# Kernel optimization log

Hardware: AMD Instinct MI355X
Metric: run time of the kernel (lower is better)

The kernel has to match this reference:

```python
import jax, jax.numpy as jnp
import numpy as np

B, H, N, D = 16, 8, 256, 32


def setup_inputs() -> dict:
    key = jax.random.key(0)
    k1, k2, k3 = jax.random.split(key, 3)
    q = jax.random.normal(k1, (B, H, N, D), dtype=jnp.float32)
    k = jax.random.normal(k2, (B, H, N, D), dtype=jnp.float32)
    scale = jnp.ones((1,), dtype=jnp.float32)  # unused by the module
    mask = jnp.zeros((B, 1, N, N), dtype=bool)  # True == masked out
    # learned attention vector, xavier_uniform over (1, H, 1, 1, D)
    fan = 1 * H * 1 * 1 * D
    bound = float(np.sqrt(6.0 / (1 + D)))  # xavier for (..., D) param
    attention = jax.random.uniform(k3, (1, H, 1, 1, D), dtype=jnp.float32,
                                   minval=-bound, maxval=bound)
    return {"q": q, "k": k, "scale": scale, "mask": mask, "attention": attention}


def reference(q, k, scale, mask, attention):
    # summed: [B, H, Nq, Nk, D] via broadcast of q.unsqueeze(-2)+k.unsqueeze(-3)
    summed = q[:, :, :, None, :] + k[:, :, None, :, :]
    # GATv2 score: a^T * silu(q_i + k_j), reduced over head_dim
    scores = jnp.sum(jax.nn.silu(summed) * attention, axis=-1)  # [B, H, Nq, Nk]
    neg = jnp.finfo(scores.dtype).min
    scores_masked = jnp.where(mask, neg, scores)
    attn = jax.nn.softmax(scores_masked, axis=-1)
    return attn
```

## Files before the change

kernel.cpp:

```cpp
#include <hip/hip_runtime.h>
#include <stdint.h>
#include <stddef.h>

constexpr int Bc = 16, Hc = 8, Nc = 256, Dc = 32;
constexpr float LOG2E = 1.44269504088896340736f;

constexpr int    MF    = 10;
constexpr double PHALF = 9.7;
constexpr double LFIT  = 9.0;

constexpr double PI_ = 3.14159265358979323846;

constexpr double cexp_(double x) {
    int n = (int)(x >= 0 ? x + 0.5 : x - 0.5);
    double f = x - n, t = 1.0, s = 1.0;
    for (int i = 1; i <= 26; ++i) { t *= f / i; s += t; }
    const double E = 2.71828182845904523536;
    double en = 1.0, bb = n >= 0 ? E : 1.0 / E;
    int an = n < 0 ? -n : n;
    for (int i = 0; i < an; ++i) en *= bb;
    return s * en;
}
constexpr double creduce_(double x) {
    while (x >  PI_) x -= 2.0 * PI_;
    while (x < -PI_) x += 2.0 * PI_;
    return x;
}
constexpr double ccos_(double x0) {
    double x = creduce_(x0), x2 = x * x, t = 1.0, s = 1.0;
    for (int i = 1; i <= 16; ++i) { t *= -x2 / ((2.0*i - 1.0) * (2.0*i)); s += t; }
    return s;
}
constexpr double csin_(double x0) {
    double x = creduce_(x0), x2 = x * x, t = x, s = x;
    for (int i = 1; i <= 16; ++i) { t *= -x2 / ((2.0*i) * (2.0*i + 1.0)); s += t; }
    return s;
}
constexpr double Gfun_(double x) {
    double z = x < 0 ? -x : x;
    double e = cexp_(z);
    return 0.5 * z * ((e - 1.0) / (e + 1.0));
}
constexpr double csqrt_(double x) {
    if (x <= 0) return 0;
    double r = x > 1 ? x : 1;
    for (int i = 0; i < 40; ++i) r = 0.5 * (r + x / r);
    return r;
}

struct FitT { float tk[MF + 1]; float tq[MF + 1]; };

constexpr FitT lsFit_() {
    constexpr int NB = MF + 1;
    double A[NB][NB] = {}, bv[NB] = {};
    for (int p = 0; p < NB; ++p)
        for (int qq = 0; qq < NB; ++qq) {
            double wm = (p - qq) * PI_ / PHALF, wp = (p + qq) * PI_ / PHALF;
            double Sm = (p == qq)     ? LFIT : csin_(wm * LFIT) / wm;
            double Sp = (p + qq == 0) ? LFIT : csin_(wp * LFIT) / wp;
            A[p][qq] = 0.5 * (Sm + Sp);
        }
    constexpr int NS = 128;
    double hh = LFIT / NS, gx[NS + 1] = {};
    for (int i = 0; i <= NS; ++i) gx[i] = Gfun_(i * hh);
    for (int p = 0; p < NB; ++p) {
        double s = 0;
        for (int i = 0; i <= NS; ++i) {
            double wgt = (i == 0 || i == NS) ? 1.0 : ((i & 1) ? 4.0 : 2.0);
            s += wgt * gx[i] * ccos_(p * PI_ / PHALF * (i * hh));
        }
        bv[p] = s * hh / 3.0;
    }
    for (int p = 0; p < NB; ++p) A[p][p] += 1e-8 * LFIT;
    for (int col = 0; col < NB; ++col) {
        int piv = col; double best = A[col][col] < 0 ? -A[col][col] : A[col][col];
        for (int r = col + 1; r < NB; ++r) {
            double v = A[r][col] < 0 ? -A[r][col] : A[r][col];
            if (v > best) { best = v; piv = r; }
        }
        if (piv != col) {
            for (int cc = 0; cc < NB; ++cc) { double t = A[col][cc]; A[col][cc] = A[piv][cc]; A[piv][cc] = t; }
            double t = bv[col]; bv[col] = bv[piv]; bv[piv] = t;
        }
        for (int r = col + 1; r < NB; ++r) {
            double f = A[r][col] / A[col][col];
            for (int cc = col; cc < NB; ++cc) A[r][cc] -= f * A[col][cc];
            bv[r] -= f * bv[col];
        }
    }
    double c[NB] = {};
    for (int r = NB - 1; r >= 0; --r) {
        double s = bv[r];
        for (int cc = r + 1; cc < NB; ++cc) s -= A[r][cc] * c[cc];
        c[r] = s / A[r][r];
    }
    FitT f{};
    for (int m = 0; m <= MF; ++m) {
        double rt = csqrt_(c[m] < 0 ? -c[m] : c[m]);
        f.tk[m] = (float)rt;
        f.tq[m] = (float)(c[m] < 0 ? -rt : rt);
    }
    return f;
}
constexpr FitT CF = lsFit_();

typedef _Float16 half8  __attribute__((ext_vector_type(8)));
typedef float    f32x16 __attribute__((ext_vector_type(16)));

__device__ __forceinline__ uint32_t pkh_(float a, float b) {
    auto v = __builtin_amdgcn_cvt_pkrtz(a, b);
    uint32_t u; __builtin_memcpy(&u, &v, 4); return u;
}

constexpr int KB_  = Nc * 128;
constexpr int QB_  = 128 * 128;
constexpr int BUF  = KB_ + QB_;
constexpr int SRED_OFF = 2 * BUF;
constexpr int AKV_OFF  = SRED_OFF + 2048;
constexpr int SMEM     = AKV_OFF + 1024;

__global__ __launch_bounds__(1024, 4) void gatv2_mfma_kernel(
    const float* __restrict__ q, const float* __restrict__ k,
    const uint8_t* __restrict__ mask, const float* __restrict__ att,
    float* __restrict__ out)
{
    extern __shared__ char smem[];
    float* sred = (float*)(smem + SRED_OFF);
    float* akv  = (float*)(smem + AKV_OFF);

    const int tid = threadIdx.x, lane = tid & 63, w = tid >> 6;
    const int bh = blockIdx.y, h = bh & 7, b = bh >> 3;
    const int iBlk = blockIdx.x * 128;
    const float invTwoP = (float)(1.0 / (2.0 * PHALF));

    const int dq = tid & 7, rw = tid >> 3;
    const float4 a4 = *(const float4*)(att + h * Dc + 4 * dq);
    const int swS = (dq ^ (rw & 7)) << 4;

    const float* kbase = k + (size_t)bh * Nc * Dc;
    float kc1[8], ks1[8], kcm[8], ksm[8];
    int offK[2];
#pragma unroll
    for (int it = 0; it < 2; ++it) {
        const int j = rw + it * 128;
        const float4 kv = *(const float4*)(kbase + j * Dc + 4 * dq);
        float part = a4.x * kv.x + a4.y * kv.y + a4.z * kv.z + a4.w * kv.w;
        part += __shfl_xor(part, 1, 64);
        part += __shfl_xor(part, 2, 64);
        part += __shfl_xor(part, 4, 64);
        if (dq == 0) akv[j] = part;
        const float rv[4] = { kv.x, kv.y, kv.z, kv.w };
#pragma unroll
        for (int c = 0; c < 4; ++c) {
            float r = __builtin_amdgcn_fractf(rv[c] * invTwoP);
            kc1[4*it+c] = __builtin_amdgcn_cosf(r);
            ks1[4*it+c] = __builtin_amdgcn_sinf(r);
            kcm[4*it+c] = kc1[4*it+c];
            ksm[4*it+c] = ks1[4*it+c];
        }
        offK[it] = j * 128 + swS;
    }
    const float* qbase = q + ((size_t)bh * Nc + iBlk) * Dc;
    float qc1[4], qs1[4], qcm[4], qsm[4];
    const int offQ = KB_ + rw * 128 + swS;
    {
        const float4 qv = *(const float4*)(qbase + rw * Dc + 4 * dq);
        const float rv[4] = { qv.x, qv.y, qv.z, qv.w };
#pragma unroll
        for (int c = 0; c < 4; ++c) {
            float r = __builtin_amdgcn_fractf(rv[c] * invTwoP);
            qc1[c] = __builtin_amdgcn_cosf(r);
            qs1[c] = __builtin_amdgcn_sinf(r);
            qcm[c] = qc1[c]; qsm[c] = qs1[c];
        }
    }

    const int hi5 = lane >> 5, col = lane & 31;
    const int wi = w & 3, wj = w >> 2;
    const int baseA  = KB_ + (wi * 32 + col) * 128;
    const int baseB0 = (wj * 64 + col) * 128, baseB1 = baseB0 + 32 * 128;
    const int sA = col & 7;

    f32x16 acc[2];
#pragma unroll
    for (int jt = 0; jt < 2; ++jt)
#pragma unroll
        for (int e = 0; e < 16; ++e) acc[jt][e] = 0.0f;

    auto buildChunk = [&](int m, int dstOff) {
        const float tk = CF.tk[m];
        const float g0 = CF.tq[m]*a4.x, g1 = CF.tq[m]*a4.y;
        const float g2 = CF.tq[m]*a4.z, g3 = CF.tq[m]*a4.w;
#pragma unroll
        for (int it = 0; it < 2; ++it) {
            uint4 wv;
            wv.x = pkh_(tk * kcm[4*it+0], tk * ksm[4*it+0]);
            wv.y = pkh_(tk * kcm[4*it+1], tk * ksm[4*it+1]);
            wv.z = pkh_(tk * kcm[4*it+2], tk * ksm[4*it+2]);
            wv.w = pkh_(tk * kcm[4*it+3], tk * ksm[4*it+3]);
            *(uint4*)(smem + dstOff + offK[it]) = wv;
        }
        {
            uint4 wv;
            wv.x = pkh_(g0 * qcm[0], -(g0 * qsm[0]));
            wv.y = pkh_(g1 * qcm[1], -(g1 * qsm[1]));
            wv.z = pkh_(g2 * qcm[2], -(g2 * qsm[2]));
            wv.w = pkh_(g3 * qcm[3], -(g3 * qsm[3]));
            *(uint4*)(smem + dstOff + offQ) = wv;
        }
        if (m < MF) {
#pragma unroll
            for (int e = 0; e < 8; ++e) {
                float cn = fmaf(kc1[e], kcm[e], -(ks1[e] * ksm[e]));
                float sn = fmaf(ks1[e], kcm[e],   kc1[e] * ksm[e]);
                kcm[e] = cn; ksm[e] = sn;
            }
#pragma unroll
            for (int e = 0; e < 4; ++e) {
                float cn = fmaf(qc1[e], qcm[e], -(qs1[e] * qsm[e]));
                float sn = fmaf(qs1[e], qcm[e],   qc1[e] * qsm[e]);
                qcm[e] = cn; qsm[e] = sn;
            }
        }
    };

    auto mfmaChunk = [&](int srcOff) {
#pragma unroll
        for (int s = 0; s < 4; ++s) {
            const int du = ((2 * s + hi5) ^ sA) << 4;
            half8 A  = *(const half8*)(smem + srcOff + baseA  + du);
            half8 B0 = *(const half8*)(smem + srcOff + baseB0 + du);
            half8 B1 = *(const half8*)(smem + srcOff + baseB1 + du);
            acc[0] = __builtin_amdgcn_mfma_f32_32x32x16_f16(A, B0, acc[0], 0, 0, 0);
            acc[1] = __builtin_amdgcn_mfma_f32_32x32x16_f16(A, B1, acc[1], 0, 0, 0);
        }
    };

    buildChunk(1, 0);
    __syncthreads();
#pragma unroll
    for (int m = 1; m <= MF; ++m) {
        if (m < MF) buildChunk(m + 1, (m & 1) * BUF);
        mfmaChunk(((m - 1) & 1) * BUF);
        __syncthreads();
    }

    constexpr float M0 = 24.0f;
    const int jB = wj * 64;
    const float akj0 = akv[jB + col], akj1 = akv[jB + 32 + col];
    const int iB = iBlk + wi * 32;

#pragma unroll
    for (int e = 0; e < 16; ++e) {
        int rloc = (e & 3) + 8 * (e >> 2) + 4 * hi5;
        int ig = iB + rloc;
        const uint8_t* mr = mask + ((size_t)(b * Nc + ig)) * Nc + jB + col;
        float v0 = fmaf(0.5f, akj0, acc[0][e]);
        float v1 = fmaf(0.5f, akj1, acc[1][e]);
        if (mr[0])  v0 = -1.0e30f;
        if (mr[32]) v1 = -1.0e30f;
        float p0 = __builtin_amdgcn_exp2f(__builtin_fminf((v0 - M0) * LOG2E, 80.0f));
        float p1 = __builtin_amdgcn_exp2f(__builtin_fminf((v1 - M0) * LOG2E, 80.0f));
        acc[0][e] = p0;
        acc[1][e] = p1;
        float sm = p0 + p1;
#pragma unroll
        for (int off = 1; off < 32; off <<= 1) sm += __shfl_xor(sm, off, 64);
        if (col == e) sred[(wi * 32 + rloc) * 4 + wj] = sm;
    }
    __syncthreads();

    float* obase = out + (size_t)bh * Nc * Nc;
#pragma unroll
    for (int e = 0; e < 16; ++e) {
        int rloc = (e & 3) + 8 * (e >> 2) + 4 * hi5;
        int iL = wi * 32 + rloc;
        int ig = iB + rloc;
        float4 tv = *(const float4*)(&sred[iL * 4]);
        float inv = __builtin_amdgcn_rcpf(tv.x + tv.y + tv.z + tv.w);
        obase[(size_t)ig * Nc + jB + col]      = acc[0][e] * inv;
        obase[(size_t)ig * Nc + jB + 32 + col] = acc[1][e] * inv;
    }
}

extern "C" void kernel_launch(void* const* d_in, const int* in_sizes, int n_in,
                              void* d_out, int out_size, void* d_ws, size_t ws_size,
                              hipStream_t stream) {
    const float*   q    = (const float*)d_in[0];
    const float*   k    = (const float*)d_in[1];
    const uint8_t* mask = (const uint8_t*)d_in[3];
    const float*   att  = (const float*)d_in[4];
    float*         out  = (float*)d_out;

    (void)hipFuncSetAttribute((const void*)gatv2_mfma_kernel,
                              hipFuncAttributeMaxDynamicSharedMemorySize, SMEM);

    dim3 grid(2, Bc * Hc);
    dim3 block(1024);
    gatv2_mfma_kernel<<<grid, block, SMEM, stream>>>(q, k, mask, att, out);
}
```

Before: 97.27 us.

## Split blocks into 64-row tiles with 512 threads and direct per-harmonic sincos

Halves the query tile per block (64 rows, 512 threads, grid 4x128) so more blocks exist and LDS per block drops. Each thread now handles four key rows. Sin/cos of each harmonic are computed directly from the fractional phase instead of through the angle-addition recurrence, which frees registers. The akv and row-sum scratch space now reuses the Q buffer after the main loop. The cost is that every K row's fp16 chunk is rebuilt by twice as many blocks, and there are more transcendental instructions per chunk.

```diff
diff --git a/kernel.cpp b/kernel.cpp
--- a/kernel.cpp
+++ b/kernel.cpp
@@ -112,25 +112,21 @@
     uint32_t u; __builtin_memcpy(&u, &v, 4); return u;
 }
 
-constexpr int KB_  = Nc * 128;
-constexpr int QB_  = 128 * 128;
-constexpr int BUF  = KB_ + QB_;
-constexpr int SRED_OFF = 2 * BUF;
-constexpr int AKV_OFF  = SRED_OFF + 2048;
-constexpr int SMEM     = AKV_OFF + 1024;
-
-__global__ __launch_bounds__(1024, 4) void gatv2_mfma_kernel(
+constexpr int KHALF = Nc * 128;
+constexpr int QOFF  = 2 * KHALF;
+constexpr int QHALF = 64 * 128;
+constexpr int SMEM  = QOFF + 2 * QHALF;
+
+__global__ __launch_bounds__(512, 4) void gatv2_mfma_kernel(
     const float* __restrict__ q, const float* __restrict__ k,
     const uint8_t* __restrict__ mask, const float* __restrict__ att,
     float* __restrict__ out)
 {
     extern __shared__ char smem[];
-    float* sred = (float*)(smem + SRED_OFF);
-    float* akv  = (float*)(smem + AKV_OFF);
 
     const int tid = threadIdx.x, lane = tid & 63, w = tid >> 6;
     const int bh = blockIdx.y, h = bh & 7, b = bh >> 3;
-    const int iBlk = blockIdx.x * 128;
+    const int iBlk = blockIdx.x * 64;
     const float invTwoP = (float)(1.0 / (2.0 * PHALF));
 
     const int dq = tid & 7, rw = tid >> 3;
@@ -138,47 +134,39 @@
     const int swS = (dq ^ (rw & 7)) << 4;
 
     const float* kbase = k + (size_t)bh * Nc * Dc;
-    float kc1[8], ks1[8], kcm[8], ksm[8];
-    int offK[2];
-#pragma unroll
-    for (int it = 0; it < 2; ++it) {
-        const int j = rw + it * 128;
+    float r1k[16], akvr[4];
+    int offK[4];
+#pragma unroll
+    for (int it = 0; it < 4; ++it) {
+        const int j = rw + it * 64;
         const float4 kv = *(const float4*)(kbase + j * Dc + 4 * dq);
         float part = a4.x * kv.x + a4.y * kv.y + a4.z * kv.z + a4.w * kv.w;
         part += __shfl_xor(part, 1, 64);
         part += __shfl_xor(part, 2, 64);
         part += __shfl_xor(part, 4, 64);
-        if (dq == 0) akv[j] = part;
+        akvr[it] = part;
         const float rv[4] = { kv.x, kv.y, kv.z, kv.w };
 #pragma unroll
-        for (int c = 0; c < 4; ++c) {
-            float r = __builtin_amdgcn_fractf(rv[c] * invTwoP);
-            kc1[4*it+c] = __builtin_amdgcn_cosf(r);
-            ks1[4*it+c] = __builtin_amdgcn_sinf(r);
-            kcm[4*it+c] = kc1[4*it+c];
-            ksm[4*it+c] = ks1[4*it+c];
-        }
+        for (int c = 0; c < 4; ++c)
+            r1k[4 * it + c] = __builtin_amdgcn_fractf(rv[c] * invTwoP);
         offK[it] = j * 128 + swS;
     }
     const float* qbase = q + ((size_t)bh * Nc + iBlk) * Dc;
-    float qc1[4], qs1[4], qcm[4], qsm[4];
-    const int offQ = KB_ + rw * 128 + swS;
+    float r1q[4];
+    const int offQ = rw * 128 + swS;
     {
         const float4 qv = *(const float4*)(qbase + rw * Dc + 4 * dq);
         const float rv[4] = { qv.x, qv.y, qv.z, qv.w };
 #pragma unroll
-        for (int c = 0; c < 4; ++c) {
-            float r = __builtin_amdgcn_fractf(rv[c] * invTwoP);
-            qc1[c] = __builtin_amdgcn_cosf(r);
-            qs1[c] = __builtin_amdgcn_sinf(r);
-            qcm[c] = qc1[c]; qsm[c] = qs1[c];
-        }
+        for (int c = 0; c < 4; ++c)
+            r1q[c] = __builtin_amdgcn_fractf(rv[c] * invTwoP);
     }
 
     const int hi5 = lane >> 5, col = lane & 31;
-    const int wi = w & 3, wj = w >> 2;
-    const int baseA  = KB_ + (wi * 32 + col) * 128;
-    const int baseB0 = (wj * 64 + col) * 128, baseB1 = baseB0 + 32 * 128;
+    const int wi = w & 1, wj = w >> 1;
+    const int baseA  = (wi * 32 + col) * 128;
+    const int baseB0 = (wj * 64 + col) * 128;
+    const int baseB1 = baseB0 + 32 * 128;
     const int sA = col & 7;
 
     f32x16 acc[2];
@@ -187,63 +175,75 @@
 #pragma unroll
         for (int e = 0; e < 16; ++e) acc[jt][e] = 0.0f;
 
-    auto buildChunk = [&](int m, int dstOff) {
+    auto buildChunk = [&](int m, int kB, int qB) {
         const float tk = CF.tk[m];
         const float g0 = CF.tq[m]*a4.x, g1 = CF.tq[m]*a4.y;
         const float g2 = CF.tq[m]*a4.z, g3 = CF.tq[m]*a4.w;
-#pragma unroll
-        for (int it = 0; it < 2; ++it) {
+        const float mf = (float)m;
+#pragma unroll
+        for (int it = 0; it < 4; ++it) {
+            float cs[4], sn[4];
+#pragma unroll
+            for (int c = 0; c < 4; ++c) {
+                const float r = __builtin_amdgcn_fractf(mf * r1k[4 * it + c]);
+                cs[c] = __builtin_amdgcn_cosf(r);
+                sn[c] = __builtin_amdgcn_sinf(r);
+            }
             uint4 wv;
-            wv.x = pkh_(tk * kcm[4*it+0], tk * ksm[4*it+0]);
-            wv.y = pkh_(tk * kcm[4*it+1], tk * ksm[4*it+1]);
-            wv.z = pkh_(tk * kcm[4*it+2], tk * ksm[4*it+2]);
-            wv.w = pkh_(tk * kcm[4*it+3], tk * ksm[4*it+3]);
-            *(uint4*)(smem + dstOff + offK[it]) = wv;
+            wv.x = pkh_(tk * cs[0], tk * sn[0]);
+            wv.y = pkh_(tk * cs[1], tk * sn[1]);
+            wv.z = pkh_(tk * cs[2], tk * sn[2]);
+            wv.w = pkh_(tk * cs[3], tk * sn[3]);
+            *(uint4*)(smem + kB + offK[it]) = wv;
         }
         {
+            float qc[4], qs[4];
+#pragma unroll
+            for (int c = 0; c < 4; ++c) {
+                const float r = __builtin_amdgcn_fractf(mf * r1q[c]);
+                qc[c] = __builtin_amdgcn_cosf(r);
+                qs[c] = __builtin_amdgcn_sinf(r);
+            }
             uint4 wv;
-            wv.x = pkh_(g0 * qcm[0], -(g0 * qsm[0]));
-            wv.y = pkh_(g1 * qcm[1], -(g1 * qsm[1]));
-            wv.z = pkh_(g2 * qcm[2], -(g2 * qsm[2]));
-            wv.w = pkh_(g3 * qcm[3], -(g3 * qsm[3]));
-            *(uint4*)(smem + dstOff + offQ) = wv;
-        }
-        if (m < MF) {
-#pragma unroll
-            for (int e = 0; e < 8; ++e) {
-                float cn = fmaf(kc1[e], kcm[e], -(ks1[e] * ksm[e]));
-                float sn = fmaf(ks1[e], kcm[e],   kc1[e] * ksm[e]);
-                kcm[e] = cn; ksm[e] = sn;
-            }
-#pragma unroll
-            for (int e = 0; e < 4; ++e) {
-                float cn = fmaf(qc1[e], qcm[e], -(qs1[e] * qsm[e]));
-                float sn = fmaf(qs1[e], qcm[e],   qc1[e] * qsm[e]);
-                qcm[e] = cn; qsm[e] = sn;
-            }
+            wv.x = pkh_(g0 * qc[0], -(g0 * qs[0]));
+            wv.y = pkh_(g1 * qc[1], -(g1 * qs[1]));
+            wv.z = pkh_(g2 * qc[2], -(g2 * qs[2]));
+            wv.w = pkh_(g3 * qc[3], -(g3 * qs[3]));
+            *(uint4*)(smem + qB + offQ) = wv;
         }
     };
 
-    auto mfmaChunk = [&](int srcOff) {
+    auto mfmaChunk = [&](int kB, int qB) {
 #pragma unroll
         for (int s = 0; s < 4; ++s) {
             const int du = ((2 * s + hi5) ^ sA) << 4;
-            half8 A  = *(const half8*)(smem + srcOff + baseA  + du);
-            half8 B0 = *(const half8*)(smem + srcOff + baseB0 + du);
-            half8 B1 = *(const half8*)(smem + srcOff + baseB1 + du);
+            half8 A  = *(const half8*)(smem + qB + baseA  + du);
+            half8 B0 = *(const half8*)(smem + kB + baseB0 + du);
+            half8 B1 = *(const half8*)(smem + kB + baseB1 + du);
             acc[0] = __builtin_amdgcn_mfma_f32_32x32x16_f16(A, B0, acc[0], 0, 0, 0);
             acc[1] = __builtin_amdgcn_mfma_f32_32x32x16_f16(A, B1, acc[1], 0, 0, 0);
         }
     };
 
-    buildChunk(1, 0);
+    buildChunk(1, 0, QOFF);
     __syncthreads();
 #pragma unroll
     for (int m = 1; m <= MF; ++m) {
-        if (m < MF) buildChunk(m + 1, (m & 1) * BUF);
-        mfmaChunk(((m - 1) & 1) * BUF);
+        const int p = (m - 1) & 1, pn = m & 1;
+        if (m < MF) buildChunk(m + 1, pn * KHALF, QOFF + pn * QHALF);
+        mfmaChunk(p * KHALF, QOFF + p * QHALF);
         __syncthreads();
     }
+
+    float* sred = (float*)(smem + QOFF);
+    float* akv  = (float*)(smem + QOFF + 1024);
+    if (dq == 0) {
+        akv[rw      ] = akvr[0];
+        akv[rw +  64] = akvr[1];
+        akv[rw + 128] = akvr[2];
+        akv[rw + 192] = akvr[3];
+    }
+    __syncthreads();
 
     constexpr float M0 = 24.0f;
     const int jB = wj * 64;
@@ -252,8 +252,8 @@
 
 #pragma unroll
     for (int e = 0; e < 16; ++e) {
-        int rloc = (e & 3) + 8 * (e >> 2) + 4 * hi5;
-        int ig = iB + rloc;
+        const int rloc = (e & 3) + 8 * (e >> 2) + 4 * hi5;
+        const int ig = iB + rloc;
         const uint8_t* mr = mask + ((size_t)(b * Nc + ig)) * Nc + jB + col;
         float v0 = fmaf(0.5f, akj0, acc[0][e]);
         float v1 = fmaf(0.5f, akj1, acc[1][e]);
@@ -273,11 +273,11 @@
     float* obase = out + (size_t)bh * Nc * Nc;
 #pragma unroll
     for (int e = 0; e < 16; ++e) {
-        int rloc = (e & 3) + 8 * (e >> 2) + 4 * hi5;
-        int iL = wi * 32 + rloc;
-        int ig = iB + rloc;
-        float4 tv = *(const float4*)(&sred[iL * 4]);
-        float inv = __builtin_amdgcn_rcpf(tv.x + tv.y + tv.z + tv.w);
+        const int rloc = (e & 3) + 8 * (e >> 2) + 4 * hi5;
+        const int iL = wi * 32 + rloc;
+        const int ig = iB + rloc;
+        const float4 tv = *(const float4*)(&sred[iL * 4]);
+        const float inv = __builtin_amdgcn_rcpf(tv.x + tv.y + tv.z + tv.w);
         obase[(size_t)ig * Nc + jB + col]      = acc[0][e] * inv;
         obase[(size_t)ig * Nc + jB + 32 + col] = acc[1][e] * inv;
     }
@@ -295,7 +295,7 @@
     (void)hipFuncSetAttribute((const void*)gatv2_mfma_kernel,
                               hipFuncAttributeMaxDynamicSharedMemorySize, SMEM);
 
-    dim3 grid(2, Bc * Hc);
-    dim3 block(1024);
+    dim3 grid(4, Bc * Hc);
+    dim3 block(512);
     gatv2_mfma_kernel<<<grid, block, SMEM, stream>>>(q, k, mask, att, out);
 }
```

Measured after the change: 103.6 us. 6.5% more time.

## Software-pipeline LDS fragment loads with MFMA and use transpose-style row-sum reduction

Applied to the files above, without the earlier changes.

The main loop now preloads the first two LDS fragment sets, builds the next chunk, then interleaves the remaining fragment loads with MFMAs under raised wave priority. It also drops the final barrier after the last chunk. The softmax row-sum reduction changes from 16 separate 5-step shuffle butterflies to a recursive halving scheme that reduces all 16 rows together with far fewer shuffles. The aim is to hide LDS latency and cut cross-lane shuffle overhead, at the cost of higher register pressure from holding two fragment sets.

```diff
diff --git a/kernel.cpp b/kernel.cpp
--- a/kernel.cpp
+++ b/kernel.cpp
@@ -187,10 +187,10 @@
 #pragma unroll
         for (int e = 0; e < 16; ++e) acc[jt][e] = 0.0f;
 
-    auto buildChunk = [&](int m, int dstOff) {
-        const float tk = CF.tk[m];
-        const float g0 = CF.tq[m]*a4.x, g1 = CF.tq[m]*a4.y;
-        const float g2 = CF.tq[m]*a4.z, g3 = CF.tq[m]*a4.w;
+    auto buildWrite = [&](int mN, int dstOff) {
+        const float tk = CF.tk[mN];
+        const float g0 = CF.tq[mN]*a4.x, g1 = CF.tq[mN]*a4.y;
+        const float g2 = CF.tq[mN]*a4.z, g3 = CF.tq[mN]*a4.w;
 #pragma unroll
         for (int it = 0; it < 2; ++it) {
             uint4 wv;
@@ -208,41 +208,52 @@
             wv.w = pkh_(g3 * qcm[3], -(g3 * qsm[3]));
             *(uint4*)(smem + dstOff + offQ) = wv;
         }
-        if (m < MF) {
-#pragma unroll
-            for (int e = 0; e < 8; ++e) {
-                float cn = fmaf(kc1[e], kcm[e], -(ks1[e] * ksm[e]));
-                float sn = fmaf(ks1[e], kcm[e],   kc1[e] * ksm[e]);
-                kcm[e] = cn; ksm[e] = sn;
-            }
-#pragma unroll
-            for (int e = 0; e < 4; ++e) {
-                float cn = fmaf(qc1[e], qcm[e], -(qs1[e] * qsm[e]));
-                float sn = fmaf(qs1[e], qcm[e],   qc1[e] * qsm[e]);
-                qcm[e] = cn; qsm[e] = sn;
-            }
-        }
     };
-
-    auto mfmaChunk = [&](int srcOff) {
-#pragma unroll
-        for (int s = 0; s < 4; ++s) {
-            const int du = ((2 * s + hi5) ^ sA) << 4;
-            half8 A  = *(const half8*)(smem + srcOff + baseA  + du);
-            half8 B0 = *(const half8*)(smem + srcOff + baseB0 + du);
-            half8 B1 = *(const half8*)(smem + srcOff + baseB1 + du);
-            acc[0] = __builtin_amdgcn_mfma_f32_32x32x16_f16(A, B0, acc[0], 0, 0, 0);
-            acc[1] = __builtin_amdgcn_mfma_f32_32x32x16_f16(A, B1, acc[1], 0, 0, 0);
+    auto rotate = [&]() {
+#pragma unroll
+        for (int e = 0; e < 8; ++e) {
+            float cn = fmaf(kc1[e], kcm[e], -(ks1[e] * ksm[e]));
+            float sn = fmaf(ks1[e], kcm[e],   kc1[e] * ksm[e]);
+            kcm[e] = cn; ksm[e] = sn;
+        }
+#pragma unroll
+        for (int e = 0; e < 4; ++e) {
+            float cn = fmaf(qc1[e], qcm[e], -(qs1[e] * qsm[e]));
+            float sn = fmaf(qs1[e], qcm[e],   qc1[e] * qsm[e]);
+            qcm[e] = cn; qsm[e] = sn;
         }
     };
-
-    buildChunk(1, 0);
+    auto loadFrags = [&](int srcOff, int s, half8& A, half8& B0, half8& B1) {
+        const int du = ((2 * s + hi5) ^ sA) << 4;
+        A  = *(const half8*)(smem + srcOff + baseA  + du);
+        B0 = *(const half8*)(smem + srcOff + baseB0 + du);
+        B1 = *(const half8*)(smem + srcOff + baseB1 + du);
+    };
+
+    buildWrite(1, 0);
+    rotate();
     __syncthreads();
 #pragma unroll
     for (int m = 1; m <= MF; ++m) {
-        if (m < MF) buildChunk(m + 1, (m & 1) * BUF);
-        mfmaChunk(((m - 1) & 1) * BUF);
-        __syncthreads();
+        const int srcOff = ((m - 1) & 1) * BUF;
+        const int dstOff = (m & 1) * BUF;
+        half8 A0, B00, B10, A1, B01, B11;
+        loadFrags(srcOff, 0, A0, B00, B10);
+        loadFrags(srcOff, 1, A1, B01, B11);
+        if (m < MF) { buildWrite(m + 1, dstOff); rotate(); }
+        __builtin_amdgcn_s_setprio(1);
+        acc[0] = __builtin_amdgcn_mfma_f32_32x32x16_f16(A0, B00, acc[0], 0, 0, 0);
+        acc[1] = __builtin_amdgcn_mfma_f32_32x32x16_f16(A0, B10, acc[1], 0, 0, 0);
+        loadFrags(srcOff, 2, A0, B00, B10);
+        acc[0] = __builtin_amdgcn_mfma_f32_32x32x16_f16(A1, B01, acc[0], 0, 0, 0);
+        acc[1] = __builtin_amdgcn_mfma_f32_32x32x16_f16(A1, B11, acc[1], 0, 0, 0);
+        loadFrags(srcOff, 3, A1, B01, B11);
+        acc[0] = __builtin_amdgcn_mfma_f32_32x32x16_f16(A0, B00, acc[0], 0, 0, 0);
+        acc[1] = __builtin_amdgcn_mfma_f32_32x32x16_f16(A0, B10, acc[1], 0, 0, 0);
+        acc[0] = __builtin_amdgcn_mfma_f32_32x32x16_f16(A1, B01, acc[0], 0, 0, 0);
+        acc[1] = __builtin_amdgcn_mfma_f32_32x32x16_f16(A1, B11, acc[1], 0, 0, 0);
+        __builtin_amdgcn_s_setprio(0);
+        if (m < MF) __syncthreads();
     }
 
     constexpr float M0 = 24.0f;
@@ -250,10 +261,11 @@
     const float akj0 = akv[jB + col], akj1 = akv[jB + 32 + col];
     const int iB = iBlk + wi * 32;
 
+    float v[16];
 #pragma unroll
     for (int e = 0; e < 16; ++e) {
-        int rloc = (e & 3) + 8 * (e >> 2) + 4 * hi5;
-        int ig = iB + rloc;
+        const int rloc = (e & 3) + 8 * (e >> 2) + 4 * hi5;
+        const int ig = iB + rloc;
         const uint8_t* mr = mask + ((size_t)(b * Nc + ig)) * Nc + jB + col;
         float v0 = fmaf(0.5f, akj0, acc[0][e]);
         float v1 = fmaf(0.5f, akj1, acc[1][e]);
@@ -263,21 +275,52 @@
         float p1 = __builtin_amdgcn_exp2f(__builtin_fminf((v1 - M0) * LOG2E, 80.0f));
         acc[0][e] = p0;
         acc[1][e] = p1;
-        float sm = p0 + p1;
-#pragma unroll
-        for (int off = 1; off < 32; off <<= 1) sm += __shfl_xor(sm, off, 64);
-        if (col == e) sred[(wi * 32 + rloc) * 4 + wj] = sm;
+        v[e] = p0 + p1;
+    }
+    float u8[8];
+#pragma unroll
+    for (int j = 0; j < 8; ++j) {
+        float mine = (col & 16) ? v[j + 8] : v[j];
+        float send = (col & 16) ? v[j]     : v[j + 8];
+        u8[j] = mine + __shfl_xor(send, 16, 64);
+    }
+    float u4[4];
+#pragma unroll
+    for (int j = 0; j < 4; ++j) {
+        float mine = (col & 8) ? u8[j + 4] : u8[j];
+        float send = (col & 8) ? u8[j]     : u8[j + 4];
+        u4[j] = mine + __shfl_xor(send, 8, 64);
+    }
+    float u2[2];
+#pragma unroll
+    for (int j = 0; j < 2; ++j) {
+        float mine = (col & 4) ? u4[j + 2] : u4[j];
+        float send = (col & 4) ? u4[j]     : u4[j + 2];
+        u2[j] = mine + __shfl_xor(send, 4, 64);
+    }
+    float t1;
+    {
+        float mine = (col & 2) ? u2[1] : u2[0];
+        float send = (col & 2) ? u2[0] : u2[1];
+        t1 = mine + __shfl_xor(send, 2, 64);
+    }
+    t1 += __shfl_xor(t1, 1, 64);
+    {
+        const int eL = ((col & 16) ? 8 : 0) + ((col & 8) ? 4 : 0)
+                     + ((col & 4) ? 2 : 0) + ((col & 2) ? 1 : 0);
+        const int rl = (eL & 3) + 8 * (eL >> 2) + 4 * hi5;
+        if (!(col & 1)) sred[(wi * 32 + rl) * 4 + wj] = t1;
     }
     __syncthreads();
 
     float* obase = out + (size_t)bh * Nc * Nc;
 #pragma unroll
     for (int e = 0; e < 16; ++e) {
-        int rloc = (e & 3) + 8 * (e >> 2) + 4 * hi5;
-        int iL = wi * 32 + rloc;
-        int ig = iB + rloc;
-        float4 tv = *(const float4*)(&sred[iL * 4]);
-        float inv = __builtin_amdgcn_rcpf(tv.x + tv.y + tv.z + tv.w);
+        const int rloc = (e & 3) + 8 * (e >> 2) + 4 * hi5;
+        const int iL = wi * 32 + rloc;
+        const int ig = iB + rloc;
+        const float4 tv = *(const float4*)(&sred[iL * 4]);
+        const float inv = __builtin_amdgcn_rcpf(tv.x + tv.y + tv.z + tv.w);
         obase[(size_t)ig * Nc + jB + col]      = acc[0][e] * inv;
         obase[(size_t)ig * Nc + jB + 32 + col] = acc[1][e] * inv;
     }
```

New measurement: 97.09 us. Within noise of the previous version (-0.2%).
